# Optimization experiments

Hardware: AMD Instinct MI355X
Metric: run time of the kernel (lower is better)

Reference implementation:

```python
import jax, jax.numpy as jnp
import numpy as np

P = 16                     # patch size
D = 192                    # embed dim (forced by SAT d_model=192)
NHEAD = 3                  # ViT-Tiny heads
SAT_H, SAT_DK, SAT_DV = 8, 32, 32
N_SLICE = 10
PER_LI = jnp.linspace(0.1, 1.0, N_SLICE)
LN_EPS = 1e-5


def layernorm(z, g, b):
    m = z.mean(-1, keepdims=True)
    v = ((z - m) ** 2).mean(-1, keepdims=True)
    return (z - m) * jax.lax.rsqrt(v + LN_EPS) * g + b


def setup_inputs() -> dict:
    key = jax.random.key(0)
    ks = jax.random.split(key, 32)
    B, IMG, DEPTH, MLP = 128, 224, 12, 4 * D
    S = (IMG // P) ** 2 + 1  # 197 tokens
    n = lambda k, sh: jax.random.normal(k, sh, jnp.float32) * 0.02
    z = lambda sh: jnp.zeros(sh, jnp.float32)
    o = lambda sh: jnp.ones(sh, jnp.float32)
    return {
        "x": jax.random.uniform(ks[0], (B, 3, IMG, IMG), jnp.float32),
        "x_g_norm": jax.random.uniform(ks[1], (B, 1, 56, 56), jnp.float32),
        "patch_w": n(ks[2], (D, 3, P, P)), "patch_b": z((D,)),
        "cls_token": n(ks[3], (1, 1, D)), "pos_embed": n(ks[4], (1, S, D)),
        "eleva_embed": n(ks[5], (1, D)),
        "sat_wq": n(ks[6], (D, SAT_H * SAT_DK)), "sat_bq": z((SAT_H * SAT_DK,)),
        "sat_wk": n(ks[7], (D, SAT_H * SAT_DK)), "sat_bk": z((SAT_H * SAT_DK,)),
        "sat_wv": n(ks[8], (D, SAT_H * SAT_DV)), "sat_bv": z((SAT_H * SAT_DV,)),
        "sat_wo": n(ks[9], (SAT_H * SAT_DV, D)), "sat_bo": z((D,)),
        "ln1_g": o((DEPTH, D)), "ln1_b": z((DEPTH, D)),
        "qkv_w": n(ks[10], (DEPTH, D, 3 * D)), "qkv_b": z((DEPTH, 3 * D)),
        "proj_w": n(ks[11], (DEPTH, D, D)), "proj_b": z((DEPTH, D)),
        "ln2_g": o((DEPTH, D)), "ln2_b": z((DEPTH, D)),
        "fc1_w": n(ks[12], (DEPTH, D, MLP)), "fc1_b": z((DEPTH, MLP)),
        "fc2_w": n(ks[13], (DEPTH, MLP, D)), "fc2_b": z((DEPTH, D)),
        "norm_g": o((D,)), "norm_b": z((D,)),
    }


def _forward(x, x_g_norm, patch_w, patch_b, cls_token, pos_embed, eleva_embed,
             sat_wq, sat_bq, sat_wk, sat_bk, sat_wv, sat_bv, sat_wo, sat_bo,
             ln1_g, ln1_b, qkv_w, qkv_b, proj_w, proj_b, ln2_g, ln2_b,
             fc1_w, fc1_b, fc2_w, fc2_b, norm_g, norm_b):
    B = x.shape[0]
    # --- patch embed: Conv2d(3, D, kernel=P, stride=P) -> [B, N, D] ---
    feat = jax.lax.conv_general_dilated(
        x, patch_w, (P, P), 'VALID', dimension_numbers=('NCHW', 'OIHW', 'NCHW'))
    feat = feat + patch_b[None, :, None, None]
    tokens = feat.reshape(B, D, -1).transpose(0, 2, 1)          # [B, 196, D]
    tok = jnp.concatenate([jnp.broadcast_to(cls_token, (B, 1, D)), tokens], axis=1)
    tok = tok + pos_embed                                        # [B, S, D]
    S = tok.shape[1]
    # --- elevation weight per sample (vectorized bisect + linear interp) ---
    means = x_g_norm.mean(axis=(1, 2, 3))                        # [B]
    idx = jnp.clip(jnp.searchsorted(PER_LI, means, side='left'), 0, N_SLICE - 1)
    per_hi = PER_LI[idx]
    per_lo = jnp.where(idx == 0, 0.0, PER_LI[jnp.maximum(idx - 1, 0)])
    idx_f = idx.astype(jnp.float32)
    idx_inter = idx_f - (per_hi - means) / (per_hi - per_lo)
    w = jnp.where(idx == N_SLICE - 1, idx_f, idx_inter) / N_SLICE  # [B]
    # --- SAT fusion: per (batch, token) a 2-element attention over (token, ele) ---
    ele = jnp.broadcast_to(eleva_embed[0] * w[:, None, None], tok.shape)  # [B,S,D]
    at_in = jnp.stack([tok, ele], axis=2)                        # [B, S, 2, D]
    q = (at_in @ sat_wq + sat_bq).reshape(B, S, 2, SAT_H, SAT_DK)
    k = (at_in @ sat_wk + sat_bk).reshape(B, S, 2, SAT_H, SAT_DK)
    v = (at_in @ sat_wv + sat_bv).reshape(B, S, 2, SAT_H, SAT_DV)
    att = jnp.einsum('bsqhd,bskhd->bshqk', q, k) * (1.0 / np.sqrt(SAT_DK))
    att = jax.nn.softmax(att, axis=-1)
    sat_o = jnp.einsum('bshqk,bskhd->bsqhd', att, v).reshape(B, S, 2, SAT_H * SAT_DV)
    sat_o = sat_o @ sat_wo + sat_bo                              # [B, S, 2, D]
    h = sat_o[..., 0, :] + sat_o[..., 1, :]                      # [B, S, D]
    # --- ViT blocks via scan over stacked layer params ---
    hd = D // NHEAD

    def block(z, p):
        l1g, l1b, qw, qb, pw, pb, l2g, l2b, f1w, f1b, f2w, f2b = p
        y = layernorm(z, l1g, l1b)
        qkv = y @ qw + qb                                        # [B, S, 3D]
        q_, k_, v_ = jnp.split(qkv, 3, axis=-1)
        q_ = q_.reshape(B, S, NHEAD, hd)
        k_ = k_.reshape(B, S, NHEAD, hd)
        v_ = v_.reshape(B, S, NHEAD, hd)
        a = jnp.einsum('bqhd,bkhd->bhqk', q_, k_) * (hd ** -0.5)
        a = jax.nn.softmax(a, axis=-1)
        o = jnp.einsum('bhqk,bkhd->bqhd', a, v_).reshape(B, S, D)
        z = z + o @ pw + pb
        y = layernorm(z, l2g, l2b)
        z = z + jax.nn.gelu(y @ f1w + f1b, approximate=False) @ f2w + f2b
        return z, None

    h, _ = jax.lax.scan(block, h, (ln1_g, ln1_b, qkv_w, qkv_b, proj_w, proj_b,
                                   ln2_g, ln2_b, fc1_w, fc1_b, fc2_w, fc2_b))
    h = layernorm(h, norm_g, norm_b)
    return h[:, 0]                                               # [B, D] cls token


def reference(x, x_g_norm, patch_w, patch_b, cls_token, pos_embed, eleva_embed,
              sat_wq, sat_bq, sat_wk, sat_bk, sat_wv, sat_bv, sat_wo, sat_bo,
              ln1_g, ln1_b, qkv_w, qkv_b, proj_w, proj_b, ln2_g, ln2_b,
              fc1_w, fc1_b, fc2_w, fc2_b, norm_g, norm_b):
    return _forward(x, x_g_norm, patch_w, patch_b, cls_token, pos_embed, eleva_embed,
                    sat_wq, sat_bq, sat_wk, sat_bk, sat_wv, sat_bv, sat_wo, sat_bo,
                    ln1_g, ln1_b, qkv_w, qkv_b, proj_w, proj_b, ln2_g, ln2_b,
                    fc1_w, fc1_b, fc2_w, fc2_b, norm_g, norm_b)
```

## Files before the change

### kernel.cpp

```cpp
#include <hip/hip_runtime.h>


#define BATCH 128
#define SEQ 197
#define BS_ROWS (BATCH * SEQ)
#define DMODEL 192
#define NPATCH 196
#define MROWS_PATCH (BATCH * NPATCH)
#define KPATCH 768
#define MLPDIM 768
#define DEPTH 12
#define SPAD 224

typedef float f32x4 __attribute__((ext_vector_type(4)));
typedef short s16x8 __attribute__((ext_vector_type(8)));

__device__ __forceinline__ float wredSum(float v) {
#pragma unroll
  for (int o = 32; o > 0; o >>= 1) v += __shfl_xor(v, o, 64);
  return v;
}

__device__ __forceinline__ unsigned short f2bf(float f) {
  union { float f; unsigned u; } v;
  v.f = f;
  unsigned r = v.u + 0x7FFFu + ((v.u >> 16) & 1u);
  return (unsigned short)(r >> 16);
}
__device__ __forceinline__ float bf2f(unsigned short u) {
  union { unsigned u; float f; } v;
  v.u = ((unsigned)u) << 16;
  return v.f;
}

__device__ __forceinline__ int swz(int col, int row) {
  int g8 = col >> 3;
  g8 = (g8 & ~7) | ((g8 & 7) ^ (row & 7));
  return (g8 << 3) | (col & 7);
}

__device__ __forceinline__ float gelu(float x) {
  const float ax = fabsf(x) * 0.70710678118654752f;
  const float t = 1.f / (1.f + 0.3275911f * ax);
  const float y =
      t * (0.254829592f +
           t * (-0.284496736f +
                t * (1.421413741f + t * (-1.453152027f + t * 1.061405429f))));
  const float erfc_ = y * __expf(-ax * ax);
  const float cdf = (x >= 0.f) ? (1.f - 0.5f * erfc_) : (0.5f * erfc_);
  return x * cdf;
}

__global__ __launch_bounds__(256) void eleva_w_kernel(const float* __restrict__ xg,
                                                      float* __restrict__ wout) {
  const int b = blockIdx.x;
  const float* p = xg + (size_t)b * 3136;
  float s = 0.f;
  for (int i = threadIdx.x; i < 3136; i += 256) s += p[i];
  __shared__ float partial[4];
  s = wredSum(s);
  if ((threadIdx.x & 63) == 0) partial[threadIdx.x >> 6] = s;
  __syncthreads();
  if (threadIdx.x == 0) {
    float m = (partial[0] + partial[1] + partial[2] + partial[3]) / 3136.f;
    int idx = 0;
#pragma unroll
    for (int i = 0; i < 10; i++) {
      float pv = 0.1f * (float)(i + 1);
      if (pv < m) idx = i + 1;
    }
    if (idx > 9) idx = 9;
    float wv;
    if (idx == 9) {
      wv = 9.f;
    } else {
      float hi = 0.1f * (float)(idx + 1);
      float lo = (idx == 0) ? 0.f : 0.1f * (float)idx;
      wv = (float)idx - (hi - m) / (hi - lo);
    }
    wout[b] = wv / 10.f;
  }
}

__global__ __launch_bounds__(256) void wtrans_kernel(const float* __restrict__ in,
                                                     unsigned short* __restrict__ out,
                                                     int R, int C) {
  const int z = blockIdx.z;
  in += (size_t)z * R * C;
  out += (size_t)z * R * C;
  const int c0 = blockIdx.x * 32, r0 = blockIdx.y * 32;
  __shared__ float t[32][33];
  const int tr = threadIdx.x >> 3, tc = (threadIdx.x & 7) * 4;
  const float4 v = *(const float4*)(in + (size_t)(r0 + tr) * C + c0 + tc);
  t[tr][tc] = v.x; t[tr][tc + 1] = v.y; t[tr][tc + 2] = v.z; t[tr][tc + 3] = v.w;
  __syncthreads();
  ushort4 o;
  o.x = f2bf(t[tc + 0][tr]);
  o.y = f2bf(t[tc + 1][tr]);
  o.z = f2bf(t[tc + 2][tr]);
  o.w = f2bf(t[tc + 3][tr]);
  const int brow = c0 + tr;
  *(ushort4*)(out + (size_t)brow * R + swz(r0 + tc, brow)) = o;
}

__global__ __launch_bounds__(256) void convert_kernel(const float* __restrict__ in,
                                                      unsigned short* __restrict__ out, int n4,
                                                      int K) {
  const int i = blockIdx.x * 256 + threadIdx.x;
  if (i >= n4) return;
  const int flat = i * 4;
  const int row = flat / K, col = flat % K;
  const float4 v = *(const float4*)(in + flat);
  ushort4 o;
  o.x = f2bf(v.x); o.y = f2bf(v.y); o.z = f2bf(v.z); o.w = f2bf(v.w);
  *(ushort4*)(out + (size_t)row * K + swz(col, row)) = o;
}

__global__ __launch_bounds__(256) void im2col_kernel(const float* __restrict__ x,
                                                     unsigned short* __restrict__ col) {
  const int i = blockIdx.x * 256 + threadIdx.x;
  if (i >= MROWS_PATCH * KPATCH / 8) return;
  const int k = (i % 96) * 8, row = i / 96;
  const int b = row / NPATCH, p = row % NPATCH;
  const int py = p / 14, px = p % 14;
  const int c = k >> 8, r = (k >> 4) & 15, cc = k & 15;
  const float* src = x + (((size_t)b * 3 + c) * 224 + (py * 16 + r)) * 224 + (px * 16 + cc);
  const float4 v0 = *(const float4*)src;
  const float4 v1 = *(const float4*)(src + 4);
  s16x8 o;
  o[0] = (short)f2bf(v0.x); o[1] = (short)f2bf(v0.y);
  o[2] = (short)f2bf(v0.z); o[3] = (short)f2bf(v0.w);
  o[4] = (short)f2bf(v1.x); o[5] = (short)f2bf(v1.y);
  o[6] = (short)f2bf(v1.z); o[7] = (short)f2bf(v1.w);
  *(s16x8*)(col + (size_t)row * KPATCH + swz(k, row)) = o;
}

__global__ __launch_bounds__(256) void cls_kernel(const float* __restrict__ cls,
                                                  const float* __restrict__ pos,
                                                  float* __restrict__ H,
                                                  unsigned short* __restrict__ Hbf) {
  const int i = blockIdx.x * 256 + threadIdx.x;
  if (i >= BATCH * DMODEL) return;
  const int b = i / DMODEL, d = i % DMODEL;
  const float v = cls[d] + pos[d];
  const int row = b * SEQ;
  H[(size_t)row * DMODEL + d] = v;
  Hbf[(size_t)row * DMODEL + swz(d, row)] = f2bf(v);
}

__global__ __launch_bounds__(256) void ele_proj_kernel(
    const float* __restrict__ ele_emb, const float* __restrict__ wq, const float* __restrict__ bq,
    const float* __restrict__ wk, const float* __restrict__ bk,
    const float* __restrict__ wv, const float* __restrict__ bv,
    const float* __restrict__ wvec, float* __restrict__ eq, float* __restrict__ ek,
    float* __restrict__ ev, float* __restrict__ satb) {
  const int b = blockIdx.x, t = threadIdx.x;
  if (b == 0) {
    satb[t] = bq[t];
    satb[256 + t] = bk[t];
    satb[512 + t] = bv[t];
  }
  __shared__ float es[DMODEL];
  if (t < DMODEL) es[t] = ele_emb[t] * wvec[b];
  __syncthreads();
  float aq = bq[t], ak = bk[t], av = bv[t];
  for (int d = 0; d < DMODEL; d++) {
    const float e = es[d];
    aq += e * wq[d * 256 + t];
    ak += e * wk[d * 256 + t];
    av += e * wv[d * 256 + t];
  }
  eq[b * 256 + t] = aq;
  ek[b * 256 + t] = ak;
  ev[b * 256 + t] = av;
}

__global__ __launch_bounds__(256) void sat_mix_kernel(
    const unsigned short* __restrict__ qkv768, const float* __restrict__ eq,
    const float* __restrict__ ek, const float* __restrict__ ev,
    unsigned short* __restrict__ o256) {
  const int gid = blockIdx.x * 256 + threadIdx.x;
  const int tok = gid >> 3, h = gid & 7;
  if (tok >= BS_ROWS) return;
  const int b = tok / SEQ;
  const unsigned short* qp = qkv768 + (size_t)tok * 768 + h * 32;
  const unsigned short* kp = qp + 256;
  const unsigned short* vp = qp + 512;
  const float* eqp = eq + b * 256 + h * 32;
  const float* ekp = ek + b * 256 + h * 32;
  const float* evp = ev + b * 256 + h * 32;
  float s00 = 0.f, s01 = 0.f, s10 = 0.f, s11 = 0.f;
#pragma unroll 8
  for (int d = 0; d < 32; d++) {
    const float q_ = bf2f(qp[d]), k_ = bf2f(kp[d]), eq_ = eqp[d], ek_ = ekp[d];
    s00 += q_ * k_;
    s01 += q_ * ek_;
    s10 += eq_ * k_;
    s11 += eq_ * ek_;
  }
  const float sc = 0.17677669529663687f;
  s00 *= sc; s01 *= sc; s10 *= sc; s11 *= sc;
  const float m0 = fmaxf(s00, s01), m1 = fmaxf(s10, s11);
  const float e00 = __expf(s00 - m0), e01 = __expf(s01 - m0);
  const float e10 = __expf(s10 - m1), e11 = __expf(s11 - m1);
  const float w0 = e00 / (e00 + e01) + e10 / (e10 + e11);
  const float w1 = e01 / (e00 + e01) + e11 / (e10 + e11);
  unsigned short* op = o256 + (size_t)tok * 256;
#pragma unroll 8
  for (int d = 0; d < 32; d++)
    op[swz(h * 32 + d, tok)] = f2bf(w0 * bf2f(vp[d]) + w1 * evp[d]);
}

template <int EPI, bool SWZO>
__global__ __launch_bounds__(256, 4) void gemm_mfma(const unsigned short* __restrict__ A,
                                                    const unsigned short* __restrict__ Bt,
                                                    const float* __restrict__ bias,
                                                    const float* __restrict__ res,
                                                    void* __restrict__ Cout,
                                                    unsigned short* __restrict__ aux_hbf,
                                                    const float* __restrict__ aux_pos,
                                                    int M, int N, int K) {
  __shared__ unsigned short As[128 * 64];
  __shared__ unsigned short Bs[96 * 64];
  const int tid = threadIdx.x, lane = tid & 63, w = tid >> 6;
  const int n0 = blockIdx.x * 96;
  const int m0 = blockIdx.y * 128;
  const int c = lane & 15, g = lane >> 4;
  const int wm = (w >> 1) * 64, wn = (w & 1) * 48;
  f32x4 acc[4][3] = {};

  const int ar = (lane >> 3);
  const int acol = (lane & 7) * 8;

  for (int k0 = 0; k0 < K; k0 += 64) {
#pragma unroll
    for (int it = 0; it < 4; it++) {
      const int r = w * 32 + it * 8 + ar;
      const unsigned short* gp = A + (size_t)(m0 + r) * K + k0 + acol;
      __builtin_amdgcn_global_load_lds(
          (const __attribute__((address_space(1))) unsigned int*)gp,
          (__attribute__((address_space(3))) unsigned int*)(As + w * 2048 + it * 512),
          16, 0, 0);
    }
#pragma unroll
    for (int it = 0; it < 3; it++) {
      const int r = w * 24 + it * 8 + ar;
      const unsigned short* gp = Bt + (size_t)(n0 + r) * K + k0 + acol;
      __builtin_amdgcn_global_load_lds(
          (const __attribute__((address_space(1))) unsigned int*)gp,
          (__attribute__((address_space(3))) unsigned int*)(Bs + w * 1536 + it * 512),
          16, 0, 0);
    }
    __syncthreads();
#pragma unroll
    for (int kk = 0; kk < 2; kk++) {
      const int sw = (((kk * 4 + g) ^ (c & 7))) << 3;
      s16x8 af[4], bfr[3];
#pragma unroll
      for (int i = 0; i < 4; i++)
        af[i] = *(const s16x8*)&As[(wm + i * 16 + c) * 64 + sw];
#pragma unroll
      for (int j = 0; j < 3; j++)
        bfr[j] = *(const s16x8*)&Bs[(wn + j * 16 + c) * 64 + sw];
#pragma unroll
      for (int i = 0; i < 4; i++)
#pragma unroll
        for (int j = 0; j < 3; j++)
          acc[i][j] = __builtin_amdgcn_mfma_f32_16x16x32_bf16(af[i], bfr[j], acc[i][j], 0, 0, 0);
    }
    __syncthreads();
  }

  const int ncol0 = n0 + wn + c;
  float bv[3];
#pragma unroll
  for (int j = 0; j < 3; j++) bv[j] = bias[ncol0 + j * 16] * (EPI == 3 ? 2.f : 1.f);
#pragma unroll
  for (int i = 0; i < 4; i++) {
#pragma unroll
    for (int r_ = 0; r_ < 4; r_++) {
      const int mrow = m0 + wm + i * 16 + g * 4 + r_;
      if (EPI == 4) {
        const int bb = mrow / 196;
        const int p = mrow - bb * 196;
        const int drow = mrow + bb + 1;
#pragma unroll
        for (int j = 0; j < 3; j++) {
          const int col = ncol0 + j * 16;
          const float v = acc[i][j][r_] + bv[j] + aux_pos[(size_t)(p + 1) * DMODEL + col];
          ((float*)Cout)[(size_t)drow * DMODEL + col] = v;
          aux_hbf[(size_t)drow * DMODEL + swz(col, drow)] = f2bf(v);
        }
      } else {
#pragma unroll
        for (int j = 0; j < 3; j++) {
          float v = acc[i][j][r_] + bv[j];
          const int col = ncol0 + j * 16;
          const size_t rowoff = (size_t)mrow * N;
          if (EPI == 0) {
            ((unsigned short*)Cout)[rowoff + (SWZO ? swz(col, mrow) : col)] = f2bf(v);
          } else if (EPI == 1) {
            ((unsigned short*)Cout)[rowoff + (SWZO ? swz(col, mrow) : col)] = f2bf(gelu(v));
          } else if (EPI == 2) {
            ((float*)Cout)[rowoff + col] = v + res[rowoff + col];
          } else {
            ((float*)Cout)[rowoff + col] = v;
          }
        }
      }
    }
  }
}

__global__ __launch_bounds__(256) void ln_kernel(const float* __restrict__ X,
                                                 const float* __restrict__ g,
                                                 const float* __restrict__ bta,
                                                 unsigned short* __restrict__ Y, int nrows) {
  const int w = threadIdx.x >> 6, lane = threadIdx.x & 63;
  const int row = blockIdx.x * 4 + w;
  if (row >= nrows) return;
  const float* x = X + (size_t)row * DMODEL;
  const float x0 = x[lane], x1 = x[lane + 64], x2 = x[lane + 128];
  const float m = wredSum(x0 + x1 + x2) * (1.f / 192.f);
  const float d0 = x0 - m, d1 = x1 - m, d2 = x2 - m;
  const float v = wredSum(d0 * d0 + d1 * d1 + d2 * d2) * (1.f / 192.f);
  const float inv = rsqrtf(v + 1e-5f);
  unsigned short* y = Y + (size_t)row * DMODEL;
  y[swz(lane, row)] = f2bf(d0 * inv * g[lane] + bta[lane]);
  y[swz(lane + 64, row)] = f2bf(d1 * inv * g[lane + 64] + bta[lane + 64]);
  y[swz(lane + 128, row)] = f2bf(d2 * inv * g[lane + 128] + bta[lane + 128]);
}

__global__ __launch_bounds__(256) void final_ln_kernel(const float* __restrict__ H,
                                                       const float* __restrict__ g,
                                                       const float* __restrict__ bta,
                                                       float* __restrict__ out) {
  const int w = threadIdx.x >> 6, lane = threadIdx.x & 63;
  const int bi = blockIdx.x * 4 + w;
  if (bi >= BATCH) return;
  const float* x = H + (size_t)bi * SEQ * DMODEL;
  const float x0 = x[lane], x1 = x[lane + 64], x2 = x[lane + 128];
  const float m = wredSum(x0 + x1 + x2) * (1.f / 192.f);
  const float d0 = x0 - m, d1 = x1 - m, d2 = x2 - m;
  const float v = wredSum(d0 * d0 + d1 * d1 + d2 * d2) * (1.f / 192.f);
  const float inv = rsqrtf(v + 1e-5f);
  float* y = out + (size_t)bi * DMODEL;
  y[lane] = d0 * inv * g[lane] + bta[lane];
  y[lane + 64] = d1 * inv * g[lane + 64] + bta[lane + 64];
  y[lane + 128] = d2 * inv * g[lane + 128] + bta[lane + 128];
}

__global__ __launch_bounds__(256) void vtrans_kernel(const unsigned short* __restrict__ qkv,
                                                     unsigned short* __restrict__ vt) {
  const int bid = blockIdx.x;
  const int sc = bid & 3, bh = bid >> 2;
  const int b = bh / 3, h = bh % 3;
  const int s0 = sc * 64;
  __shared__ unsigned short t[64][72];
  const int tid = threadIdx.x;
  for (int e = tid; e < 64 * 64; e += 256) {
    const int sp = e >> 6, d = e & 63;
    const int s = s0 + sp;
    t[sp][d] = (s < SEQ) ? qkv[((size_t)(b * SEQ + s)) * 576 + 384 + h * 64 + d] : (unsigned short)0;
  }
  __syncthreads();
  for (int e = tid; e < 64 * 64; e += 256) {
    const int d = e >> 6, sp = e & 63;
    const int s = s0 + sp;
    if (s < SPAD) vt[((size_t)bh * 64 + d) * SPAD + s] = t[sp][d];
  }
}

__global__ __launch_bounds__(64) void attn_mfma_kernel(const unsigned short* __restrict__ qkv,
                                                       const unsigned short* __restrict__ vt,
                                                       unsigned short* __restrict__ out) {
  const int bid = blockIdx.x;
  const int bh = bid / 13, qt = bid % 13;
  const int b = bh / 3, h = bh % 3;
  const int row0 = b * SEQ;
  const int q0 = qt * 16;
  const int lane = threadIdx.x;
  const int c = lane & 15, g = lane >> 4;

  __shared__ __attribute__((aligned(16))) unsigned short P[16][232];

  const int qr = row0 + min(q0 + c, SEQ - 1);
  const unsigned short* qp = qkv + (size_t)qr * 576 + h * 64 + g * 8;
  const s16x8 qlo = *(const s16x8*)qp;
  const s16x8 qhi = *(const s16x8*)(qp + 32);

  f32x4 acc[13];
#pragma unroll
  for (int t = 0; t < 13; t++) {
    const int kr = row0 + min(t * 16 + c, SEQ - 1);
    const unsigned short* kp = qkv + (size_t)kr * 576 + 192 + h * 64 + g * 8;
    const s16x8 klo = *(const s16x8*)kp;
    const s16x8 khi = *(const s16x8*)(kp + 32);
    f32x4 z = {0.f, 0.f, 0.f, 0.f};
    z = __builtin_amdgcn_mfma_f32_16x16x32_bf16(qlo, klo, z, 0, 0, 0);
    acc[t] = __builtin_amdgcn_mfma_f32_16x16x32_bf16(qhi, khi, z, 0, 0, 0);
  }

  const bool m12 = (c >= 5);
#pragma unroll
  for (int r = 0; r < 4; r++) {
    float mx = -INFINITY;
#pragma unroll
    for (int t = 0; t < 13; t++) {
      const float v = (t == 12 && m12) ? -INFINITY : acc[t][r];
      mx = fmaxf(mx, v);
    }
#pragma unroll
    for (int o = 1; o <= 8; o <<= 1) mx = fmaxf(mx, __shfl_xor(mx, o, 64));
    const float ms = mx * 0.125f;
    float sum = 0.f;
#pragma unroll
    for (int t = 0; t < 13; t++) {
      const float e = (t == 12 && m12) ? 0.f : __expf(acc[t][r] * 0.125f - ms);
      acc[t][r] = e;
      sum += e;
    }
#pragma unroll
    for (int o = 1; o <= 8; o <<= 1) sum += __shfl_xor(sum, o, 64);
    const float inv = 1.f / sum;
#pragma unroll
    for (int t = 0; t < 13; t++) P[g * 4 + r][t * 16 + c] = f2bf(acc[t][r] * inv);
  }
  {
    unsigned short z4[4] = {0, 0, 0, 0};
    *(uint2*)&P[c][208 + g * 4] = *(uint2*)z4;
  }
  __builtin_amdgcn_s_waitcnt(0);

  f32x4 oacc[4];
#pragma unroll
  for (int dt = 0; dt < 4; dt++) oacc[dt] = (f32x4){0.f, 0.f, 0.f, 0.f};
  const unsigned short* vbase = vt + (size_t)bh * 64 * SPAD;
#pragma unroll
  for (int ch = 0; ch < 7; ch++) {
    const s16x8 pa = *(const s16x8*)&P[c][ch * 32 + g * 8];
#pragma unroll
    for (int dt = 0; dt < 4; dt++) {
      const s16x8 vb = *(const s16x8*)(vbase + (size_t)(dt * 16 + c) * SPAD + ch * 32 + g * 8);
      oacc[dt] = __builtin_amdgcn_mfma_f32_16x16x32_bf16(pa, vb, oacc[dt], 0, 0, 0);
    }
  }

#pragma unroll
  for (int dt = 0; dt < 4; dt++) {
#pragma unroll
    for (int r = 0; r < 4; r++) {
      const int q = q0 + g * 4 + r;
      if (q < SEQ) {
        const int trow = row0 + q;
        out[(size_t)trow * DMODEL + swz(h * 64 + dt * 16 + c, trow)] = f2bf(oacc[dt][r]);
      }
    }
  }
}

extern "C" void kernel_launch(void* const* d_in, const int* in_sizes, int n_in,
                              void* d_out, int out_size, void* d_ws, size_t ws_size,
                              hipStream_t stream) {
  const float* x       = (const float*)d_in[0];
  const float* xg      = (const float*)d_in[1];
  const float* patch_w = (const float*)d_in[2];
  const float* patch_b = (const float*)d_in[3];
  const float* cls_tok = (const float*)d_in[4];
  const float* pos_emb = (const float*)d_in[5];
  const float* ele_emb = (const float*)d_in[6];
  const float* sat_wq  = (const float*)d_in[7];
  const float* sat_bq  = (const float*)d_in[8];
  const float* sat_wk  = (const float*)d_in[9];
  const float* sat_bk  = (const float*)d_in[10];
  const float* sat_wv  = (const float*)d_in[11];
  const float* sat_bv  = (const float*)d_in[12];
  const float* sat_wo  = (const float*)d_in[13];
  const float* sat_bo  = (const float*)d_in[14];
  const float* ln1_g   = (const float*)d_in[15];
  const float* ln1_b   = (const float*)d_in[16];
  const float* qkv_w   = (const float*)d_in[17];
  const float* qkv_b   = (const float*)d_in[18];
  const float* proj_w  = (const float*)d_in[19];
  const float* proj_b  = (const float*)d_in[20];
  const float* ln2_g   = (const float*)d_in[21];
  const float* ln2_b   = (const float*)d_in[22];
  const float* fc1_w   = (const float*)d_in[23];
  const float* fc1_b   = (const float*)d_in[24];
  const float* fc2_w   = (const float*)d_in[25];
  const float* fc2_b   = (const float*)d_in[26];
  const float* norm_g  = (const float*)d_in[27];
  const float* norm_b  = (const float*)d_in[28];
  float* out = (float*)d_out;
  float* ws = (float*)d_ws;

  float* W_ELE = ws;
  float* EQ = ws + 256;
  float* EK = EQ + 32768;
  float* EV = EK + 32768;
  float* H = ws + 98560;
  unsigned short* Hbf   = (unsigned short*)(ws + 4940032);
  unsigned short* Ybf   = (unsigned short*)(ws + 7360768);
  unsigned short* QKVbf = (unsigned short*)(ws + 9781504);
  unsigned short* MLPbf = (unsigned short*)(ws + 17043712);
  unsigned short* VTB   = (unsigned short*)(ws + 26726656);
  unsigned short* WTS   = (unsigned short*)(ws + 29479168);
  float* SATB = ws + 32305408;

  unsigned short* qkv_wt   = WTS;
  unsigned short* proj_wt  = WTS + 1327104;
  unsigned short* fc1_wt   = WTS + 1769472;
  unsigned short* fc2_wt   = WTS + 3538944;
  unsigned short* patch_bf = WTS + 5308416;
  unsigned short* satqkv_t = WTS + 5455872;
  unsigned short* sato_t   = WTS + 5603328;

  unsigned short* COLbf   = MLPbf;
  unsigned short* SATQKV  = MLPbf;
  unsigned short* O256bf  = QKVbf;

  wtrans_kernel<<<dim3(18, 6, 12), 256, 0, stream>>>(qkv_w, qkv_wt, 192, 576);
  wtrans_kernel<<<dim3(6, 6, 12), 256, 0, stream>>>(proj_w, proj_wt, 192, 192);
  wtrans_kernel<<<dim3(24, 6, 12), 256, 0, stream>>>(fc1_w, fc1_wt, 192, 768);
  wtrans_kernel<<<dim3(6, 24, 12), 256, 0, stream>>>(fc2_w, fc2_wt, 768, 192);
  wtrans_kernel<<<dim3(8, 6, 1), 256, 0, stream>>>(sat_wq, satqkv_t, 192, 256);
  wtrans_kernel<<<dim3(8, 6, 1), 256, 0, stream>>>(sat_wk, satqkv_t + 49152, 192, 256);
  wtrans_kernel<<<dim3(8, 6, 1), 256, 0, stream>>>(sat_wv, satqkv_t + 98304, 192, 256);
  wtrans_kernel<<<dim3(6, 8, 1), 256, 0, stream>>>(sat_wo, sato_t, 256, 192);
  convert_kernel<<<144, 256, 0, stream>>>(patch_w, patch_bf, 36864, KPATCH);

  eleva_w_kernel<<<BATCH, 256, 0, stream>>>(xg, W_ELE);

  im2col_kernel<<<(MROWS_PATCH * KPATCH / 8) / 256, 256, 0, stream>>>(x, COLbf);
  gemm_mfma<4, false><<<dim3(2, 196), 256, 0, stream>>>(COLbf, patch_bf, patch_b, nullptr, H,
                                                        Hbf, pos_emb, MROWS_PATCH, DMODEL,
                                                        KPATCH);
  cls_kernel<<<(BATCH * DMODEL) / 256, 256, 0, stream>>>(cls_tok, pos_emb, H, Hbf);

  ele_proj_kernel<<<BATCH, 256, 0, stream>>>(ele_emb, sat_wq, sat_bq, sat_wk, sat_bk,
                                             sat_wv, sat_bv, W_ELE, EQ, EK, EV, SATB);
  gemm_mfma<0, false><<<dim3(8, 197), 256, 0, stream>>>(Hbf, satqkv_t, SATB, nullptr, SATQKV,
                                                        nullptr, nullptr, BS_ROWS, 768, DMODEL);
  sat_mix_kernel<<<BS_ROWS / 32, 256, 0, stream>>>(SATQKV, EQ, EK, EV, O256bf);
  gemm_mfma<3, false><<<dim3(2, 197), 256, 0, stream>>>(O256bf, sato_t, sat_bo, nullptr, H,
                                                        nullptr, nullptr, BS_ROWS, DMODEL, 256);

  for (int l = 0; l < DEPTH; l++) {
    ln_kernel<<<BS_ROWS / 4, 256, 0, stream>>>(H, ln1_g + l * DMODEL, ln1_b + l * DMODEL, Ybf,
                                               BS_ROWS);
    gemm_mfma<0, false><<<dim3(6, 197), 256, 0, stream>>>(Ybf, qkv_wt + (size_t)l * 110592,
                                                          qkv_b + l * 576, nullptr, QKVbf,
                                                          nullptr, nullptr, BS_ROWS, 576,
                                                          DMODEL);
    vtrans_kernel<<<BATCH * 3 * 4, 256, 0, stream>>>(QKVbf, VTB);
    attn_mfma_kernel<<<BATCH * 3 * 13, 64, 0, stream>>>(QKVbf, VTB, Ybf);
    gemm_mfma<2, false><<<dim3(2, 197), 256, 0, stream>>>(Ybf, proj_wt + (size_t)l * 36864,
                                                          proj_b + l * DMODEL, H, H, nullptr,
                                                          nullptr, BS_ROWS, DMODEL, DMODEL);
    ln_kernel<<<BS_ROWS / 4, 256, 0, stream>>>(H, ln2_g + l * DMODEL, ln2_b + l * DMODEL, Ybf,
                                               BS_ROWS);
    gemm_mfma<1, true><<<dim3(8, 197), 256, 0, stream>>>(Ybf, fc1_wt + (size_t)l * 147456,
                                                         fc1_b + l * MLPDIM, nullptr, MLPbf,
                                                         nullptr, nullptr, BS_ROWS, MLPDIM,
                                                         DMODEL);
    gemm_mfma<2, false><<<dim3(2, 197), 256, 0, stream>>>(MLPbf, fc2_wt + (size_t)l * 147456,
                                                          fc2_b + l * DMODEL, H, H, nullptr,
                                                          nullptr, BS_ROWS, DMODEL, MLPDIM);
  }

  final_ln_kernel<<<BATCH / 4, 256, 0, stream>>>(H, norm_g, norm_b, out);
}
```

Measured before the change: 1.819 ms.

## Fuse LayerNorm into N=192 GEMM epilogues and vectorize SAT mix

Adds a BN=192 GEMM variant in which each block owns full 192-column rows. The residual-add epilogue now computes the row statistics via shuffles and shared memory and writes the normalized bf16 activations for the next layer, so the standalone LayerNorm kernels and their reread of H disappear. The attention output goes to a separate buffer because Ybf is now written by the fused epilogue. The SAT mix kernel switches to 16-byte vector loads and stores. The cost is a larger per-block register and LDS footprint and fewer blocks (launch bound 1) for the N=192 GEMMs, plus a one-pass E[x²]−mean² variance that is less numerically robust.

```diff
diff --git a/kernel.cpp b/kernel.cpp
--- a/kernel.cpp
+++ b/kernel.cpp
@@ -184,19 +184,32 @@
   if (tok >= BS_ROWS) return;
   const int b = tok / SEQ;
   const unsigned short* qp = qkv768 + (size_t)tok * 768 + h * 32;
-  const unsigned short* kp = qp + 256;
-  const unsigned short* vp = qp + 512;
-  const float* eqp = eq + b * 256 + h * 32;
-  const float* ekp = ek + b * 256 + h * 32;
-  const float* evp = ev + b * 256 + h * 32;
+  s16x8 qv[4], kv[4];
+#pragma unroll
+  for (int i0 = 0; i0 < 4; i0++) {
+    qv[i0] = *(const s16x8*)(qp + i0 * 8);
+    kv[i0] = *(const s16x8*)(qp + 256 + i0 * 8);
+  }
+  float eqa[32], eka[32];
+  {
+    const float4* eqp = (const float4*)(eq + b * 256 + h * 32);
+    const float4* ekp = (const float4*)(ek + b * 256 + h * 32);
+#pragma unroll
+    for (int i0 = 0; i0 < 8; i0++) {
+      const float4 a = eqp[i0], c = ekp[i0];
+      eqa[i0 * 4] = a.x; eqa[i0 * 4 + 1] = a.y; eqa[i0 * 4 + 2] = a.z; eqa[i0 * 4 + 3] = a.w;
+      eka[i0 * 4] = c.x; eka[i0 * 4 + 1] = c.y; eka[i0 * 4 + 2] = c.z; eka[i0 * 4 + 3] = c.w;
+    }
+  }
   float s00 = 0.f, s01 = 0.f, s10 = 0.f, s11 = 0.f;
-#pragma unroll 8
+#pragma unroll
   for (int d = 0; d < 32; d++) {
-    const float q_ = bf2f(qp[d]), k_ = bf2f(kp[d]), eq_ = eqp[d], ek_ = ekp[d];
+    const float q_ = bf2f((unsigned short)qv[d >> 3][d & 7]);
+    const float k_ = bf2f((unsigned short)kv[d >> 3][d & 7]);
     s00 += q_ * k_;
-    s01 += q_ * ek_;
-    s10 += eq_ * k_;
-    s11 += eq_ * ek_;
+    s01 += q_ * eka[d];
+    s10 += eqa[d] * k_;
+    s11 += eqa[d] * eka[d];
   }
   const float sc = 0.17677669529663687f;
   s00 *= sc; s01 *= sc; s10 *= sc; s11 *= sc;
@@ -206,28 +219,43 @@
   const float w0 = e00 / (e00 + e01) + e10 / (e10 + e11);
   const float w1 = e01 / (e00 + e01) + e11 / (e10 + e11);
   unsigned short* op = o256 + (size_t)tok * 256;
-#pragma unroll 8
-  for (int d = 0; d < 32; d++)
-    op[swz(h * 32 + d, tok)] = f2bf(w0 * bf2f(vp[d]) + w1 * evp[d]);
-}
-
-template <int EPI, bool SWZO>
-__global__ __launch_bounds__(256, 4) void gemm_mfma(const unsigned short* __restrict__ A,
-                                                    const unsigned short* __restrict__ Bt,
-                                                    const float* __restrict__ bias,
-                                                    const float* __restrict__ res,
-                                                    void* __restrict__ Cout,
-                                                    unsigned short* __restrict__ aux_hbf,
-                                                    const float* __restrict__ aux_pos,
-                                                    int M, int N, int K) {
+  const float4* evp = (const float4*)(ev + b * 256 + h * 32);
+#pragma unroll
+  for (int i0 = 0; i0 < 4; i0++) {
+    const s16x8 vv = *(const s16x8*)(qp + 512 + i0 * 8);
+    const float4 e0 = evp[i0 * 2], e1 = evp[i0 * 2 + 1];
+    float ev8[8] = {e0.x, e0.y, e0.z, e0.w, e1.x, e1.y, e1.z, e1.w};
+    s16x8 o;
+#pragma unroll
+    for (int e = 0; e < 8; e++)
+      o[e] = (short)f2bf(w0 * bf2f((unsigned short)vv[e]) + w1 * ev8[e]);
+    *(s16x8*)(op + swz(h * 32 + i0 * 8, tok)) = o;
+  }
+}
+
+template <int EPI, bool SWZO, int BN>
+__global__ __launch_bounds__(256, (BN == 96) ? 4 : 1)
+void gemm_mfma(const unsigned short* __restrict__ A,
+               const unsigned short* __restrict__ Bt,
+               const float* __restrict__ bias,
+               const float* __restrict__ res,
+               void* __restrict__ Cout,
+               unsigned short* __restrict__ aux_hbf,
+               const float* __restrict__ aux_pos,
+               const float* __restrict__ lng,
+               const float* __restrict__ lnb,
+               int M, int N, int K) {
+  constexpr int NJ = BN / 32;
+  constexpr bool LNF = (EPI == 5 || EPI == 6);
   __shared__ unsigned short As[128 * 64];
-  __shared__ unsigned short Bs[96 * 64];
+  __shared__ unsigned short Bs[BN * 64];
+  __shared__ float2 lnbuf[2][128];
   const int tid = threadIdx.x, lane = tid & 63, w = tid >> 6;
-  const int n0 = blockIdx.x * 96;
+  const int n0 = blockIdx.x * BN;
   const int m0 = blockIdx.y * 128;
   const int c = lane & 15, g = lane >> 4;
-  const int wm = (w >> 1) * 64, wn = (w & 1) * 48;
-  f32x4 acc[4][3] = {};
+  const int wm = (w >> 1) * 64, wn = (w & 1) * (BN / 2);
+  f32x4 acc[4][NJ] = {};
 
   const int ar = (lane >> 3);
   const int acol = (lane & 7) * 8;
@@ -243,92 +271,120 @@
           16, 0, 0);
     }
 #pragma unroll
-    for (int it = 0; it < 3; it++) {
-      const int r = w * 24 + it * 8 + ar;
+    for (int it = 0; it < NJ; it++) {
+      const int r = w * (BN / 4) + it * 8 + ar;
       const unsigned short* gp = Bt + (size_t)(n0 + r) * K + k0 + acol;
       __builtin_amdgcn_global_load_lds(
           (const __attribute__((address_space(1))) unsigned int*)gp,
-          (__attribute__((address_space(3))) unsigned int*)(Bs + w * 1536 + it * 512),
+          (__attribute__((address_space(3))) unsigned int*)(Bs + (w * (BN / 4) + it * 8) * 64),
           16, 0, 0);
     }
     __syncthreads();
 #pragma unroll
     for (int kk = 0; kk < 2; kk++) {
       const int sw = (((kk * 4 + g) ^ (c & 7))) << 3;
-      s16x8 af[4], bfr[3];
+      s16x8 af[4], bfr[NJ];
 #pragma unroll
       for (int i = 0; i < 4; i++)
         af[i] = *(const s16x8*)&As[(wm + i * 16 + c) * 64 + sw];
 #pragma unroll
-      for (int j = 0; j < 3; j++)
+      for (int j = 0; j < NJ; j++)
         bfr[j] = *(const s16x8*)&Bs[(wn + j * 16 + c) * 64 + sw];
 #pragma unroll
       for (int i = 0; i < 4; i++)
 #pragma unroll
-        for (int j = 0; j < 3; j++)
+        for (int j = 0; j < NJ; j++)
           acc[i][j] = __builtin_amdgcn_mfma_f32_16x16x32_bf16(af[i], bfr[j], acc[i][j], 0, 0, 0);
     }
     __syncthreads();
   }
 
   const int ncol0 = n0 + wn + c;
-  float bv[3];
-#pragma unroll
-  for (int j = 0; j < 3; j++) bv[j] = bias[ncol0 + j * 16] * (EPI == 3 ? 2.f : 1.f);
-#pragma unroll
-  for (int i = 0; i < 4; i++) {
-#pragma unroll
-    for (int r_ = 0; r_ < 4; r_++) {
-      const int mrow = m0 + wm + i * 16 + g * 4 + r_;
-      if (EPI == 4) {
-        const int bb = mrow / 196;
-        const int p = mrow - bb * 196;
-        const int drow = mrow + bb + 1;
-#pragma unroll
-        for (int j = 0; j < 3; j++) {
+  float bv[NJ];
+#pragma unroll
+  for (int j = 0; j < NJ; j++) bv[j] = bias[ncol0 + j * 16] * (EPI == 6 ? 2.f : 1.f);
+
+  if constexpr (LNF) {
+    const int p = w & 1;
+#pragma unroll
+    for (int i = 0; i < 4; i++) {
+#pragma unroll
+      for (int r_ = 0; r_ < 4; r_++) {
+        const int lr = wm + i * 16 + g * 4 + r_;
+        const int mrow = m0 + lr;
+        float s1 = 0.f, s2 = 0.f;
+#pragma unroll
+        for (int j = 0; j < NJ; j++) {
+          float v = acc[i][j][r_] + bv[j];
+          if (EPI == 5) v += res[(size_t)mrow * DMODEL + ncol0 + j * 16];
+          acc[i][j][r_] = v;
+          ((float*)Cout)[(size_t)mrow * DMODEL + ncol0 + j * 16] = v;
+          s1 += v;
+          s2 += v * v;
+        }
+#pragma unroll
+        for (int o = 1; o <= 8; o <<= 1) {
+          s1 += __shfl_xor(s1, o, 64);
+          s2 += __shfl_xor(s2, o, 64);
+        }
+        if (c == 0) lnbuf[p][lr] = make_float2(s1, s2);
+      }
+    }
+    __syncthreads();
+    float lg[NJ], lb[NJ];
+#pragma unroll
+    for (int j = 0; j < NJ; j++) { lg[j] = lng[ncol0 + j * 16]; lb[j] = lnb[ncol0 + j * 16]; }
+#pragma unroll
+    for (int i = 0; i < 4; i++) {
+#pragma unroll
+      for (int r_ = 0; r_ < 4; r_++) {
+        const int lr = wm + i * 16 + g * 4 + r_;
+        const int mrow = m0 + lr;
+        const float2 a0 = lnbuf[0][lr], a1 = lnbuf[1][lr];
+        const float mean = (a0.x + a1.x) * (1.f / 192.f);
+        const float var = (a0.y + a1.y) * (1.f / 192.f) - mean * mean;
+        const float inv = rsqrtf(var + 1e-5f);
+#pragma unroll
+        for (int j = 0; j < NJ; j++) {
           const int col = ncol0 + j * 16;
-          const float v = acc[i][j][r_] + bv[j] + aux_pos[(size_t)(p + 1) * DMODEL + col];
-          ((float*)Cout)[(size_t)drow * DMODEL + col] = v;
-          aux_hbf[(size_t)drow * DMODEL + swz(col, drow)] = f2bf(v);
+          const float yn = (acc[i][j][r_] - mean) * inv * lg[j] + lb[j];
+          aux_hbf[(size_t)mrow * DMODEL + swz(col, mrow)] = f2bf(yn);
         }
-      } else {
-#pragma unroll
-        for (int j = 0; j < 3; j++) {
-          float v = acc[i][j][r_] + bv[j];
-          const int col = ncol0 + j * 16;
-          const size_t rowoff = (size_t)mrow * N;
-          if (EPI == 0) {
-            ((unsigned short*)Cout)[rowoff + (SWZO ? swz(col, mrow) : col)] = f2bf(v);
-          } else if (EPI == 1) {
-            ((unsigned short*)Cout)[rowoff + (SWZO ? swz(col, mrow) : col)] = f2bf(gelu(v));
-          } else if (EPI == 2) {
-            ((float*)Cout)[rowoff + col] = v + res[rowoff + col];
-          } else {
-            ((float*)Cout)[rowoff + col] = v;
+      }
+    }
+  } else {
+#pragma unroll
+    for (int i = 0; i < 4; i++) {
+#pragma unroll
+      for (int r_ = 0; r_ < 4; r_++) {
+        const int mrow = m0 + wm + i * 16 + g * 4 + r_;
+        if (EPI == 4) {
+          const int bb = mrow / 196;
+          const int p = mrow - bb * 196;
+          const int drow = mrow + bb + 1;
+#pragma unroll
+          for (int j = 0; j < NJ; j++) {
+            const int col = ncol0 + j * 16;
+            const float v = acc[i][j][r_] + bv[j] + aux_pos[(size_t)(p + 1) * DMODEL + col];
+            ((float*)Cout)[(size_t)drow * DMODEL + col] = v;
+            aux_hbf[(size_t)drow * DMODEL + swz(col, drow)] = f2bf(v);
+          }
+        } else {
+#pragma unroll
+          for (int j = 0; j < NJ; j++) {
+            float v = acc[i][j][r_] + bv[j];
+            const int col = ncol0 + j * 16;
+            const size_t rowoff = (size_t)mrow * N;
+            if (EPI == 0) {
+              ((unsigned short*)Cout)[rowoff + (SWZO ? swz(col, mrow) : col)] = f2bf(v);
+            } else {
+              ((unsigned short*)Cout)[rowoff + (SWZO ? swz(col, mrow) : col)] = f2bf(gelu(v));
+            }
           }
         }
       }
     }
   }
-}
-
-__global__ __launch_bounds__(256) void ln_kernel(const float* __restrict__ X,
-                                                 const float* __restrict__ g,
-                                                 const float* __restrict__ bta,
-                                                 unsigned short* __restrict__ Y, int nrows) {
-  const int w = threadIdx.x >> 6, lane = threadIdx.x & 63;
-  const int row = blockIdx.x * 4 + w;
-  if (row >= nrows) return;
-  const float* x = X + (size_t)row * DMODEL;
-  const float x0 = x[lane], x1 = x[lane + 64], x2 = x[lane + 128];
-  const float m = wredSum(x0 + x1 + x2) * (1.f / 192.f);
-  const float d0 = x0 - m, d1 = x1 - m, d2 = x2 - m;
-  const float v = wredSum(d0 * d0 + d1 * d1 + d2 * d2) * (1.f / 192.f);
-  const float inv = rsqrtf(v + 1e-5f);
-  unsigned short* y = Y + (size_t)row * DMODEL;
-  y[swz(lane, row)] = f2bf(d0 * inv * g[lane] + bta[lane]);
-  y[swz(lane + 64, row)] = f2bf(d1 * inv * g[lane + 64] + bta[lane + 64]);
-  y[swz(lane + 128, row)] = f2bf(d2 * inv * g[lane + 128] + bta[lane + 128]);
 }
 
 __global__ __launch_bounds__(256) void final_ln_kernel(const float* __restrict__ H,
@@ -506,6 +562,7 @@
   unsigned short* VTB   = (unsigned short*)(ws + 26726656);
   unsigned short* WTS   = (unsigned short*)(ws + 29479168);
   float* SATB = ws + 32305408;
+  unsigned short* ATTNbf = (unsigned short*)(ws + 32306176);
 
   unsigned short* qkv_wt   = WTS;
   unsigned short* proj_wt  = WTS + 1327104;
@@ -532,40 +589,38 @@
   eleva_w_kernel<<<BATCH, 256, 0, stream>>>(xg, W_ELE);
 
   im2col_kernel<<<(MROWS_PATCH * KPATCH / 8) / 256, 256, 0, stream>>>(x, COLbf);
-  gemm_mfma<4, false><<<dim3(2, 196), 256, 0, stream>>>(COLbf, patch_bf, patch_b, nullptr, H,
-                                                        Hbf, pos_emb, MROWS_PATCH, DMODEL,
-                                                        KPATCH);
+  gemm_mfma<4, false, 96><<<dim3(2, 196), 256, 0, stream>>>(
+      COLbf, patch_bf, patch_b, nullptr, H, Hbf, pos_emb, nullptr, nullptr,
+      MROWS_PATCH, DMODEL, KPATCH);
   cls_kernel<<<(BATCH * DMODEL) / 256, 256, 0, stream>>>(cls_tok, pos_emb, H, Hbf);
 
   ele_proj_kernel<<<BATCH, 256, 0, stream>>>(ele_emb, sat_wq, sat_bq, sat_wk, sat_bk,
                                              sat_wv, sat_bv, W_ELE, EQ, EK, EV, SATB);
-  gemm_mfma<0, false><<<dim3(8, 197), 256, 0, stream>>>(Hbf, satqkv_t, SATB, nullptr, SATQKV,
-                                                        nullptr, nullptr, BS_ROWS, 768, DMODEL);
+  gemm_mfma<0, false, 96><<<dim3(8, 197), 256, 0, stream>>>(
+      Hbf, satqkv_t, SATB, nullptr, SATQKV, nullptr, nullptr, nullptr, nullptr,
+      BS_ROWS, 768, DMODEL);
   sat_mix_kernel<<<BS_ROWS / 32, 256, 0, stream>>>(SATQKV, EQ, EK, EV, O256bf);
-  gemm_mfma<3, false><<<dim3(2, 197), 256, 0, stream>>>(O256bf, sato_t, sat_bo, nullptr, H,
-                                                        nullptr, nullptr, BS_ROWS, DMODEL, 256);
+  gemm_mfma<6, false, 192><<<dim3(1, 197), 256, 0, stream>>>(
+      O256bf, sato_t, sat_bo, nullptr, H, Ybf, nullptr, ln1_g, ln1_b,
+      BS_ROWS, DMODEL, 256);
 
   for (int l = 0; l < DEPTH; l++) {
-    ln_kernel<<<BS_ROWS / 4, 256, 0, stream>>>(H, ln1_g + l * DMODEL, ln1_b + l * DMODEL, Ybf,
-                                               BS_ROWS);
-    gemm_mfma<0, false><<<dim3(6, 197), 256, 0, stream>>>(Ybf, qkv_wt + (size_t)l * 110592,
-                                                          qkv_b + l * 576, nullptr, QKVbf,
-                                                          nullptr, nullptr, BS_ROWS, 576,
-                                                          DMODEL);
+    gemm_mfma<0, false, 96><<<dim3(6, 197), 256, 0, stream>>>(
+        Ybf, qkv_wt + (size_t)l * 110592, qkv_b + l * 576, nullptr, QKVbf, nullptr, nullptr,
+        nullptr, nullptr, BS_ROWS, 576, DMODEL);
     vtrans_kernel<<<BATCH * 3 * 4, 256, 0, stream>>>(QKVbf, VTB);
-    attn_mfma_kernel<<<BATCH * 3 * 13, 64, 0, stream>>>(QKVbf, VTB, Ybf);
-    gemm_mfma<2, false><<<dim3(2, 197), 256, 0, stream>>>(Ybf, proj_wt + (size_t)l * 36864,
-                                                          proj_b + l * DMODEL, H, H, nullptr,
-                                                          nullptr, BS_ROWS, DMODEL, DMODEL);
-    ln_kernel<<<BS_ROWS / 4, 256, 0, stream>>>(H, ln2_g + l * DMODEL, ln2_b + l * DMODEL, Ybf,
-                                               BS_ROWS);
-    gemm_mfma<1, true><<<dim3(8, 197), 256, 0, stream>>>(Ybf, fc1_wt + (size_t)l * 147456,
-                                                         fc1_b + l * MLPDIM, nullptr, MLPbf,
-                                                         nullptr, nullptr, BS_ROWS, MLPDIM,
-                                                         DMODEL);
-    gemm_mfma<2, false><<<dim3(2, 197), 256, 0, stream>>>(MLPbf, fc2_wt + (size_t)l * 147456,
-                                                          fc2_b + l * DMODEL, H, H, nullptr,
-                                                          nullptr, BS_ROWS, DMODEL, MLPDIM);
+    attn_mfma_kernel<<<BATCH * 3 * 13, 64, 0, stream>>>(QKVbf, VTB, ATTNbf);
+    gemm_mfma<5, false, 192><<<dim3(1, 197), 256, 0, stream>>>(
+        ATTNbf, proj_wt + (size_t)l * 36864, proj_b + l * DMODEL, H, H, Ybf, nullptr,
+        ln2_g + l * DMODEL, ln2_b + l * DMODEL, BS_ROWS, DMODEL, DMODEL);
+    gemm_mfma<1, true, 96><<<dim3(8, 197), 256, 0, stream>>>(
+        Ybf, fc1_wt + (size_t)l * 147456, fc1_b + l * MLPDIM, nullptr, MLPbf, nullptr, nullptr,
+        nullptr, nullptr, BS_ROWS, MLPDIM, DMODEL);
+    const float* nlg = (l < DEPTH - 1) ? (ln1_g + (l + 1) * DMODEL) : norm_g;
+    const float* nlb = (l < DEPTH - 1) ? (ln1_b + (l + 1) * DMODEL) : norm_b;
+    gemm_mfma<5, false, 192><<<dim3(1, 197), 256, 0, stream>>>(
+        MLPbf, fc2_wt + (size_t)l * 147456, fc2_b + l * DMODEL, H, H, Ybf, nullptr,
+        nlg, nlb, BS_ROWS, DMODEL, MLPDIM);
   }
 
   final_ln_kernel<<<BATCH / 4, 256, 0, stream>>>(H, norm_g, norm_b, out);
```

New measurement: 1.890 ms. 3.9% more time.
